# Optimization experiments

Hardware: AMD Instinct MI355X
Metric: run time of the kernel (lower is better)

The kernel has to match this reference:

```python
import jax, jax.numpy as jnp
import numpy as np

N_NODES = 50000   # batch_size * num_nodes
N_EDGES = 800000
D_IN = 128
D_OUT = 128


def setup_inputs() -> dict:
    key = jax.random.key(0)
    k1, k2, k3, k4 = jax.random.split(key, 4)
    x = jax.random.normal(k1, (N_NODES, D_IN), dtype=jnp.float32)
    edge_index = jax.random.randint(k2, (2, N_EDGES), 0, N_NODES, dtype=jnp.int64)
    W = jax.random.normal(k3, (D_OUT, D_IN), dtype=jnp.float32) * (1.0 / np.sqrt(D_IN))
    b = jax.random.normal(k4, (D_OUT,), dtype=jnp.float32) * 0.01
    return {"x": x, "edge_index": edge_index, "batch_size": 50, "num_nodes": 1000, "W": W, "b": b}


def reference(x, edge_index, batch_size, num_nodes, W, b):
    dim_size = batch_size * num_nodes
    row, col = edge_index[0], edge_index[1]
    # gather messages and segment-mean aggregate over destination rows
    msgs = x[col]                                   # [E, D_IN]
    summed = jax.ops.segment_sum(msgs, row, num_segments=dim_size)      # [N, D_IN]
    counts = jax.ops.segment_sum(jnp.ones((row.shape[0],), dtype=x.dtype), row,
                                 num_segments=dim_size)                 # [N]
    mean = summed / jnp.maximum(counts, 1.0)[:, None]                   # 0 for empty rows
    # linear projection (torch Linear: y = x @ W.T + b)
    return mean @ W.T + b
```

## Files before the change

### kernel.cpp

```cpp
#include <hip/hip_runtime.h>

#define D 128
#define BSHIFT 6
#define BCAP 1536
#define EPB_A 2048

typedef unsigned short ushort_t;
typedef unsigned int uint_t;
typedef __attribute__((ext_vector_type(8))) short short8_t;
typedef __attribute__((ext_vector_type(4))) float f32x4_t;

__device__ __forceinline__ bool eidx_is64(const int* eidx) {
    int lane = threadIdx.x & 63;
    int probe = eidx[2 * lane + 1];
    return __ballot(probe != 0) == 0ULL;
}

__device__ __forceinline__ uint_t f2bf(float f) {
    union { float f; uint_t i; } v; v.f = f;
    return (v.i + 0x7fffu + ((v.i >> 16) & 1u)) >> 16;
}
__device__ __forceinline__ float bf_lo(uint_t w) {
    union { uint_t i; float f; } v; v.i = w << 16; return v.f;
}
__device__ __forceinline__ float bf_hi(uint_t w) {
    union { uint_t i; float f; } v; v.i = w & 0xffff0000u; return v.f;
}

__global__ __launch_bounds__(256) void bucketA_kernel(
    const int* __restrict__ eidx, int* __restrict__ gcur,
    int* __restrict__ bucket, int E, int NBUK) {
    __shared__ int lhist[1024];
    __shared__ int lbase[1024];
    bool is64 = eidx_is64(eidx);
    int t = threadIdx.x;
    for (int i = t; i < NBUK; i += 256) lhist[i] = 0;
    __syncthreads();

    int e0 = blockIdx.x * EPB_A;
    int e1 = min(e0 + EPB_A, E);
    for (int e = e0 + t; e < e1; e += 256) {
        int r = is64 ? eidx[2 * e] : eidx[e];
        atomicAdd(&lhist[r >> BSHIFT], 1);
    }
    __syncthreads();
    for (int i = t; i < NBUK; i += 256) {
        int h = lhist[i];
        lbase[i] = (h > 0) ? atomicAdd(&gcur[i], h) : 0;
        lhist[i] = 0;
    }
    __syncthreads();
    for (int e = e0 + t; e < e1; e += 256) {
        int r, c;
        if (is64) { r = eidx[2 * e]; c = eidx[2 * E + 2 * e]; }
        else      { r = eidx[e];     c = eidx[E + e]; }
        int b = r >> BSHIFT;
        int p = atomicAdd(&lhist[b], 1);
        int idx = lbase[b] + p;
        if (idx < BCAP) bucket[b * BCAP + idx] = ((r & 63) << 24) | c;
    }
}

__global__ __launch_bounds__(256) void prep_kernel(
    const int* __restrict__ gcur, const int* __restrict__ bucket,
    int* __restrict__ elist, int* __restrict__ cnt,
    int* __restrict__ start, int N, int NBUK,
    const float* __restrict__ x, uint_t* __restrict__ xb, int total8, int cvb,
    const float* __restrict__ Wsrc, uint_t* __restrict__ wb) {
    __shared__ int lcnt[64], lpos[64], lstart[64];
    int t = threadIdx.x;

    if ((int)blockIdx.x >= NBUK) {
        if (xb == nullptr) return;
        int cb = blockIdx.x - NBUK;
        if (cb < cvb) {
            int i = cb * 256 + t;
            if (i < total8) {
                const float4* p = (const float4*)(x + (size_t)i * 8);
                float4 a = p[0], b = p[1];
                uint4 o;
                o.x = f2bf(a.x) | (f2bf(a.y) << 16);
                o.y = f2bf(a.z) | (f2bf(a.w) << 16);
                o.z = f2bf(b.x) | (f2bf(b.y) << 16);
                o.w = f2bf(b.z) | (f2bf(b.w) << 16);
                *(uint4*)(xb + (size_t)i * 4) = o;
            }
            if (cb == 0 && t < 16) {
                uint4 z; z.x = 0u; z.y = 0u; z.z = 0u; z.w = 0u;
                ((uint4*)(xb + (size_t)N * (D / 2)))[t] = z;
            }
        } else {
            int i = (cb - cvb) * 256 + t;
            if (i < D * D / 8) {
                const float4* p = (const float4*)(Wsrc + (size_t)i * 8);
                float4 a = p[0], b = p[1];
                uint4 o;
                o.x = f2bf(a.x) | (f2bf(a.y) << 16);
                o.y = f2bf(a.z) | (f2bf(a.w) << 16);
                o.z = f2bf(b.x) | (f2bf(b.y) << 16);
                o.w = f2bf(b.z) | (f2bf(b.w) << 16);
                *(uint4*)(wb + (size_t)i * 4) = o;
            }
        }
        return;
    }

    int b = blockIdx.x;
    if (t < 64) { lcnt[t] = 0; lpos[t] = 0; }
    __syncthreads();
    int tot = min(gcur[b], BCAP);
    const int* bp = bucket + (size_t)b * BCAP;
    for (int i = t; i < tot; i += 256)
        atomicAdd(&lcnt[bp[i] >> 24], 1);
    __syncthreads();
    if (t == 0) {
        int run = 0;
        #pragma unroll
        for (int i = 0; i < 64; ++i) {
            lstart[i] = run;
            run += (lcnt[i] + 7) & ~7;
        }
    }
    __syncthreads();
    for (int i = t; i < tot; i += 256) {
        int v = bp[i];
        int rl = v >> 24;
        int p = atomicAdd(&lpos[rl], 1);
        int idx = lstart[rl] + p;
        if (idx < BCAP) elist[(size_t)b * BCAP + idx] = v & 0xFFFFFF;
    }
    if (t < 64) {
        int gr = (b << BSHIFT) + t;
        int c0 = lcnt[t];
        int pe = (c0 + 7) & ~7;
        for (int p = c0; p < pe; ++p) {
            int idx = lstart[t] + p;
            if (idx < BCAP) elist[(size_t)b * BCAP + idx] = N;
        }
        if (gr < N) { cnt[gr] = c0; start[gr] = b * BCAP + lstart[t]; }
    }
}

#define GATHER8(CA, CB)                                                       \
    {                                                                         \
        uint4 g0 = *(const uint4*)(xs + (size_t)(CA).x * D);                  \
        uint4 g1 = *(const uint4*)(xs + (size_t)(CA).y * D);                  \
        uint4 g2 = *(const uint4*)(xs + (size_t)(CA).z * D);                  \
        uint4 g3 = *(const uint4*)(xs + (size_t)(CA).w * D);                  \
        uint4 g4 = *(const uint4*)(xs + (size_t)(CB).x * D);                  \
        uint4 g5 = *(const uint4*)(xs + (size_t)(CB).y * D);                  \
        uint4 g6 = *(const uint4*)(xs + (size_t)(CB).z * D);                  \
        uint4 g7 = *(const uint4*)(xs + (size_t)(CB).w * D);                  \
        a0 += ((bf_lo(g0.x) + bf_lo(g1.x)) + (bf_lo(g2.x) + bf_lo(g3.x)))     \
            + ((bf_lo(g4.x) + bf_lo(g5.x)) + (bf_lo(g6.x) + bf_lo(g7.x)));    \
        a1 += ((bf_hi(g0.x) + bf_hi(g1.x)) + (bf_hi(g2.x) + bf_hi(g3.x)))     \
            + ((bf_hi(g4.x) + bf_hi(g5.x)) + (bf_hi(g6.x) + bf_hi(g7.x)));    \
        a2 += ((bf_lo(g0.y) + bf_lo(g1.y)) + (bf_lo(g2.y) + bf_lo(g3.y)))     \
            + ((bf_lo(g4.y) + bf_lo(g5.y)) + (bf_lo(g6.y) + bf_lo(g7.y)));    \
        a3 += ((bf_hi(g0.y) + bf_hi(g1.y)) + (bf_hi(g2.y) + bf_hi(g3.y)))     \
            + ((bf_hi(g4.y) + bf_hi(g5.y)) + (bf_hi(g6.y) + bf_hi(g7.y)));    \
        a4 += ((bf_lo(g0.z) + bf_lo(g1.z)) + (bf_lo(g2.z) + bf_lo(g3.z)))     \
            + ((bf_lo(g4.z) + bf_lo(g5.z)) + (bf_lo(g6.z) + bf_lo(g7.z)));    \
        a5 += ((bf_hi(g0.z) + bf_hi(g1.z)) + (bf_hi(g2.z) + bf_hi(g3.z)))     \
            + ((bf_hi(g4.z) + bf_hi(g5.z)) + (bf_hi(g6.z) + bf_hi(g7.z)));    \
        a6 += ((bf_lo(g0.w) + bf_lo(g1.w)) + (bf_lo(g2.w) + bf_lo(g3.w)))     \
            + ((bf_lo(g4.w) + bf_lo(g5.w)) + (bf_lo(g6.w) + bf_lo(g7.w)));    \
        a7 += ((bf_hi(g0.w) + bf_hi(g1.w)) + (bf_hi(g2.w) + bf_hi(g3.w)))     \
            + ((bf_hi(g4.w) + bf_hi(g5.w)) + (bf_hi(g6.w) + bf_hi(g7.w)));    \
    }

__global__ __launch_bounds__(256, 6) void fused_bf_kernel(
    const ushort_t* __restrict__ xb, const int* __restrict__ elist,
    const int* __restrict__ cnt, const int* __restrict__ start,
    const ushort_t* __restrict__ Wb, const float* __restrict__ bias,
    float* __restrict__ out, int N) {
    __shared__ ushort_t sA[32 * 136];
    int t = threadIdx.x;
    int lane = t & 63, wave = t >> 6;
    int qr = lane >> 4, sl = lane & 15;
    int nbase = blockIdx.x * 32;
    const ushort_t* xs = xb + 8 * sl;

    #pragma unroll
    for (int quad = 0; quad < 2; ++quad) {
        int n = wave * 8 + quad * 4 + qr;
        int gn = nbase + n;
        int nr  = (gn < N) ? cnt[gn]   : 0;
        int beg = (gn < N) ? start[gn] : 0;
        int nr8 = (nr + 7) & ~7;
        int mn = nr8;
        mn = min(mn, __shfl_xor(mn, 16));
        mn = min(mn, __shfl_xor(mn, 32));
        float a0 = 0.f, a1 = 0.f, a2 = 0.f, a3 = 0.f;
        float a4 = 0.f, a5 = 0.f, a6 = 0.f, a7 = 0.f;
        const int* ep = elist + beg;
        int4 cA, cB;
        if (nr8 > 0) { cA = *(const int4*)ep; cB = *(const int4*)(ep + 4); }
        int i = 0;
        for (; i < mn; ) {
            int ni = i + 8;
            int4 nA2, nB2;
            if (ni < nr8) {
                nA2 = *(const int4*)(ep + ni);
                nB2 = *(const int4*)(ep + ni + 4);
            }
            GATHER8(cA, cB)
            cA = nA2; cB = nB2; i = ni;
        }
        for (; i < nr8; i += 8) {
            int4 dA = *(const int4*)(ep + i);
            int4 dB = *(const int4*)(ep + i + 4);
            GATHER8(dA, dB)
        }
        float inv = (nr > 0) ? 1.0f / (float)nr : 0.0f;
        uint4 pk;
        pk.x = f2bf(a0 * inv) | (f2bf(a1 * inv) << 16);
        pk.y = f2bf(a2 * inv) | (f2bf(a3 * inv) << 16);
        pk.z = f2bf(a4 * inv) | (f2bf(a5 * inv) << 16);
        pk.w = f2bf(a6 * inv) | (f2bf(a7 * inv) << 16);
        *(uint4*)(sA + n * 136 + 8 * sl) = pk;
    }
    __syncthreads();

    {
        int rt = wave & 1, jgrp = wave >> 1;
        int ml = lane & 15, kh = lane >> 4;
        short8_t afr[4];
        #pragma unroll
        for (int ks = 0; ks < 4; ++ks)
            afr[ks] = *(const short8_t*)(sA + (rt * 16 + ml) * 136 + ks * 32 + kh * 8);
        f32x4_t acc[4];
        #pragma unroll
        for (int q = 0; q < 4; ++q) acc[q] = (f32x4_t){0.f, 0.f, 0.f, 0.f};
        #pragma unroll
        for (int q = 0; q < 4; ++q) {
            int j = (jgrp * 4 + q) * 16 + ml;
            #pragma unroll
            for (int ks = 0; ks < 4; ++ks) {
                short8_t bfr = *(const short8_t*)(Wb + (size_t)j * D + ks * 32 + kh * 8);
                acc[q] = __builtin_amdgcn_mfma_f32_16x16x32_bf16(afr[ks], bfr, acc[q], 0, 0, 0);
            }
        }
        #pragma unroll
        for (int q = 0; q < 4; ++q) {
            int j = (jgrp * 4 + q) * 16 + ml;
            float bj = bias[j];
            #pragma unroll
            for (int r = 0; r < 4; ++r) {
                int gn = nbase + rt * 16 + kh * 4 + r;
                if (gn < N) out[(size_t)gn * D + j] = acc[q][r] + bj;
            }
        }
    }
}

__global__ __launch_bounds__(256, 6) void fused_kernel(
    const float* __restrict__ x, const int* __restrict__ elist,
    const int* __restrict__ cnt, const int* __restrict__ start,
    const float* __restrict__ W, const float* __restrict__ bias,
    float* __restrict__ out, int N) {
    __shared__ float sT[128 * 36];
    __shared__ float wc[16 * 132];
    int t = threadIdx.x;
    int lane = t & 63, wave = t >> 6;
    int half = lane >> 5, sl = lane & 31;
    int nbase = blockIdx.x * 32;

    #pragma unroll
    for (int pair = 0; pair < 4; ++pair) {
        int n = wave * 8 + pair * 2 + half;
        int gn = nbase + n;
        int nr  = (gn < N) ? cnt[gn]   : 0;
        int beg = (gn < N) ? start[gn] : 0;
        int nro  = __shfl(nr, lane ^ 32);
        int both = min(nr, nro);
        float ax = 0.f, ay = 0.f, az = 0.f, aw = 0.f;
        int i = 0;
        for (; i + 8 <= both; i += 8) {
            int4 cA = *(const int4*)(elist + beg + i);
            int4 cB = *(const int4*)(elist + beg + i + 4);
            float4 v0 = *(const float4*)(x + (size_t)cA.x * D + 4 * sl);
            float4 v1 = *(const float4*)(x + (size_t)cA.y * D + 4 * sl);
            float4 v2 = *(const float4*)(x + (size_t)cA.z * D + 4 * sl);
            float4 v3 = *(const float4*)(x + (size_t)cA.w * D + 4 * sl);
            float4 v4 = *(const float4*)(x + (size_t)cB.x * D + 4 * sl);
            float4 v5 = *(const float4*)(x + (size_t)cB.y * D + 4 * sl);
            float4 v6 = *(const float4*)(x + (size_t)cB.z * D + 4 * sl);
            float4 v7 = *(const float4*)(x + (size_t)cB.w * D + 4 * sl);
            ax += ((v0.x + v1.x) + (v2.x + v3.x)) + ((v4.x + v5.x) + (v6.x + v7.x));
            ay += ((v0.y + v1.y) + (v2.y + v3.y)) + ((v4.y + v5.y) + (v6.y + v7.y));
            az += ((v0.z + v1.z) + (v2.z + v3.z)) + ((v4.z + v5.z) + (v6.z + v7.z));
            aw += ((v0.w + v1.w) + (v2.w + v3.w)) + ((v4.w + v5.w) + (v6.w + v7.w));
        }
        for (; i < nr; ++i) {
            int c0 = elist[beg + i];
            float4 v = *(const float4*)(x + (size_t)c0 * D + 4 * sl);
            ax += v.x; ay += v.y; az += v.z; aw += v.w;
        }
        float inv = (nr > 0) ? 1.0f / (float)nr : 0.0f;
        int k0 = 4 * sl;
        sT[(k0 + 0) * 36 + n] = ax * inv;
        sT[(k0 + 1) * 36 + n] = ay * inv;
        sT[(k0 + 2) * 36 + n] = az * inv;
        sT[(k0 + 3) * 36 + n] = aw * inv;
    }

    int jg = t & 31, ng = t >> 5;
    int j0 = jg * 4, n0 = ng * 4;
    float acc[4][4] = {};
    for (int kc = 0; kc < 8; ++kc) {
        __syncthreads();
        #pragma unroll
        for (int i = 0; i < 8; ++i) {
            int idx = t + i * 256;
            int j = idx >> 4, kk = idx & 15;
            wc[kk * 132 + j] = W[j * D + kc * 16 + kk];
        }
        __syncthreads();
        #pragma unroll
        for (int kk = 0; kk < 16; ++kk) {
            int k = kc * 16 + kk;
            float4 s4 = *(const float4*)(sT + k * 36 + n0);
            float4 w4 = *(const float4*)(wc + kk * 132 + j0);
            acc[0][0] = fmaf(s4.x, w4.x, acc[0][0]); acc[0][1] = fmaf(s4.x, w4.y, acc[0][1]);
            acc[0][2] = fmaf(s4.x, w4.z, acc[0][2]); acc[0][3] = fmaf(s4.x, w4.w, acc[0][3]);
            acc[1][0] = fmaf(s4.y, w4.x, acc[1][0]); acc[1][1] = fmaf(s4.y, w4.y, acc[1][1]);
            acc[1][2] = fmaf(s4.y, w4.z, acc[1][2]); acc[1][3] = fmaf(s4.y, w4.w, acc[1][3]);
            acc[2][0] = fmaf(s4.z, w4.x, acc[2][0]); acc[2][1] = fmaf(s4.z, w4.y, acc[2][1]);
            acc[2][2] = fmaf(s4.z, w4.z, acc[2][2]); acc[2][3] = fmaf(s4.z, w4.w, acc[2][3]);
            acc[3][0] = fmaf(s4.w, w4.x, acc[3][0]); acc[3][1] = fmaf(s4.w, w4.y, acc[3][1]);
            acc[3][2] = fmaf(s4.w, w4.z, acc[3][2]); acc[3][3] = fmaf(s4.w, w4.w, acc[3][3]);
        }
    }
    float4 b4 = *(const float4*)(bias + j0);
    #pragma unroll
    for (int i = 0; i < 4; ++i) {
        int gn = nbase + n0 + i;
        if (gn >= N) continue;
        float4 o;
        o.x = acc[i][0] + b4.x;
        o.y = acc[i][1] + b4.y;
        o.z = acc[i][2] + b4.z;
        o.w = acc[i][3] + b4.w;
        *(float4*)(out + (size_t)gn * D + j0) = o;
    }
}

__global__ __launch_bounds__(256) void scatter_kernel(
    const float* __restrict__ x, const int* __restrict__ eidx,
    float* summed, float* __restrict__ counts, int E) {
    int t = blockIdx.x * 256 + threadIdx.x;
    int lane = threadIdx.x & 63;
    bool is64 = eidx_is64(eidx);
    int e = t >> 6;
    if (e >= E) return;
    int d = lane * 2;
    int r, c;
    if (is64) { r = eidx[2 * e]; c = eidx[2 * E + 2 * e]; }
    else      { r = eidx[e];     c = eidx[E + e]; }
    float2 v = *(const float2*)(x + (size_t)c * D + d);
    float* dst = summed + (size_t)r * D + d;
    atomicAdd(dst, v.x);
    atomicAdd(dst + 1, v.y);
    if (lane == 0) atomicAdd(counts + r, 1.0f);
}

__global__ __launch_bounds__(256) void divide_kernel(
    float* __restrict__ sums, const float* __restrict__ counts, int N) {
    int g = blockIdx.x * 256 + threadIdx.x;
    int r = g >> 6, lane = g & 63;
    if (r >= N) return;
    float inv = 1.0f / fmaxf(counts[r], 1.0f);
    float2* p = (float2*)(sums + (size_t)r * D + 2 * lane);
    float2 v = *p;
    v.x *= inv; v.y *= inv;
    *p = v;
}

__global__ __launch_bounds__(256) void gemm_kernel(
    float* inout, const float* __restrict__ W,
    const float* __restrict__ bias, int N) {
    __shared__ float sT[128 * 36];
    __shared__ float wc[32 * 132];
    int t = threadIdx.x;
    int nbase = blockIdx.x * 32;
    #pragma unroll
    for (int i = 0; i < 16; ++i) {
        int idx = t + i * 256;
        int n = idx >> 7, k = idx & 127;
        int gn = nbase + n;
        sT[k * 36 + n] = (gn < N) ? inout[(size_t)gn * D + k] : 0.0f;
    }
    int jg = t & 31, ng = t >> 5;
    int j0 = jg * 4, n0 = ng * 4;
    float acc[4][4] = {};
    for (int kc = 0; kc < 4; ++kc) {
        __syncthreads();
        #pragma unroll
        for (int i = 0; i < 16; ++i) {
            int idx = t + i * 256;
            int j = idx >> 5, kk = idx & 31;
            wc[kk * 132 + j] = W[j * D + kc * 32 + kk];
        }
        __syncthreads();
        #pragma unroll 8
        for (int kk = 0; kk < 32; ++kk) {
            int k = kc * 32 + kk;
            float4 s4 = *(const float4*)(sT + k * 36 + n0);
            float4 w4 = *(const float4*)(wc + kk * 132 + j0);
            acc[0][0] = fmaf(s4.x, w4.x, acc[0][0]); acc[0][1] = fmaf(s4.x, w4.y, acc[0][1]);
            acc[0][2] = fmaf(s4.x, w4.z, acc[0][2]); acc[0][3] = fmaf(s4.x, w4.w, acc[0][3]);
            acc[1][0] = fmaf(s4.y, w4.x, acc[1][0]); acc[1][1] = fmaf(s4.y, w4.y, acc[1][1]);
            acc[1][2] = fmaf(s4.y, w4.z, acc[1][2]); acc[1][3] = fmaf(s4.y, w4.w, acc[1][3]);
            acc[2][0] = fmaf(s4.z, w4.x, acc[2][0]); acc[2][1] = fmaf(s4.z, w4.y, acc[2][1]);
            acc[2][2] = fmaf(s4.z, w4.z, acc[2][2]); acc[2][3] = fmaf(s4.z, w4.w, acc[2][3]);
            acc[3][0] = fmaf(s4.w, w4.x, acc[3][0]); acc[3][1] = fmaf(s4.w, w4.y, acc[3][1]);
            acc[3][2] = fmaf(s4.w, w4.z, acc[3][2]); acc[3][3] = fmaf(s4.w, w4.w, acc[3][3]);
        }
    }
    float4 b4 = *(const float4*)(bias + j0);
    #pragma unroll
    for (int i = 0; i < 4; ++i) {
        int gn = nbase + n0 + i;
        if (gn >= N) continue;
        float4 o;
        o.x = acc[i][0] + b4.x;
        o.y = acc[i][1] + b4.y;
        o.z = acc[i][2] + b4.z;
        o.w = acc[i][3] + b4.w;
        *(float4*)(inout + (size_t)gn * D + j0) = o;
    }
}

extern "C" void kernel_launch(void* const* d_in, const int* in_sizes, int n_in,
                              void* d_out, int out_size, void* d_ws, size_t ws_size,
                              hipStream_t stream) {
    const float* x = (const float*)d_in[0];
    const int* eidx = (const int*)d_in[1];
    const float* W = (const float*)d_in[4];
    const float* b = (const float*)d_in[5];
    float* out = (float*)d_out;

    int N = in_sizes[0] / D;
    int E = in_sizes[1] / 2;
    int NBUK = (N + 63) >> BSHIFT;
    int fb = (N + 31) / 32;
    int ab = (E + EPB_A - 1) / EPB_A;

    size_t o0 = 0;
    size_t o_gc = o0;  o0 += ((size_t)NBUK * 4 + 255) & ~255ULL;
    size_t o_cn = o0;  o0 += ((size_t)N * 4 + 255) & ~255ULL;
    size_t o_st = o0;  o0 += ((size_t)N * 4 + 255) & ~255ULL;
    size_t o_bk = o0;  o0 += (size_t)NBUK * BCAP * 4;
    size_t o_el = o0;  o0 += (size_t)NBUK * BCAP * 4;
    size_t base_need = o0;
    size_t o_xb = o0;  o0 += (((size_t)(N + 1) * D * 2) + 255) & ~255ULL;
    size_t o_wb = o0;  size_t bf_need = o0 + (size_t)D * D * 2;

    bool cap_ok = (N <= 65536) && ((size_t)NBUK * BCAP >= (size_t)E);

    int cvb = (N * D / 8 + 255) / 256;
    int wvb = (D * D / 8 + 255) / 256;

    if (cap_ok && ws_size >= bf_need) {
        char* ws = (char*)d_ws;
        int*      gcur  = (int*)(ws + o_gc);
        int*      cnt   = (int*)(ws + o_cn);
        int*      start = (int*)(ws + o_st);
        int*      bkt   = (int*)(ws + o_bk);
        int*      elist = (int*)(ws + o_el);
        ushort_t* xb    = (ushort_t*)(ws + o_xb);
        ushort_t* wb    = (ushort_t*)(ws + o_wb);

        hipMemsetAsync(gcur, 0, (size_t)NBUK * 4, stream);
        bucketA_kernel<<<ab, 256, 0, stream>>>(eidx, gcur, bkt, E, NBUK);
        prep_kernel<<<NBUK + cvb + wvb, 256, 0, stream>>>(
            gcur, bkt, elist, cnt, start, N, NBUK,
            x, (uint_t*)xb, N * D / 8, cvb, W, (uint_t*)wb);
        fused_bf_kernel<<<fb, 256, 0, stream>>>(xb, elist, cnt, start, wb, b, out, N);
    } else if (cap_ok && ws_size >= base_need) {
        char* ws = (char*)d_ws;
        int* gcur  = (int*)(ws + o_gc);
        int* cnt   = (int*)(ws + o_cn);
        int* start = (int*)(ws + o_st);
        int* bkt   = (int*)(ws + o_bk);
        int* elist = (int*)(ws + o_el);

        hipMemsetAsync(gcur, 0, (size_t)NBUK * 4, stream);
        bucketA_kernel<<<ab, 256, 0, stream>>>(eidx, gcur, bkt, E, NBUK);
        prep_kernel<<<NBUK, 256, 0, stream>>>(
            gcur, bkt, elist, cnt, start, N, NBUK,
            nullptr, nullptr, 0, 0, nullptr, nullptr);
        fused_kernel<<<fb, 256, 0, stream>>>(x, elist, cnt, start, W, b, out, N);
    } else {
        float* counts = (float*)d_ws;
        hipMemsetAsync(d_out, 0, (size_t)N * D * sizeof(float), stream);
        hipMemsetAsync(d_ws, 0, (size_t)N * sizeof(float), stream);
        int sb = (E * 64 + 255) / 256;
        scatter_kernel<<<sb, 256, 0, stream>>>(x, eidx, out, counts, E);
        int db = (N * 64 + 255) / 256;
        divide_kernel<<<db, 256, 0, stream>>>(out, counts, N);
        gemm_kernel<<<fb, 256, 0, stream>>>(out, W, b, N);
    }
}
```

Measured before the change: 164.5 us.

## Widen gather to 16 edges per iteration and cache edge indices in bucketing

The aggregation loop now gathers 16 neighbor rows per iteration instead of 8, with a per-lane prefetch of the next 16 indices. The launch-bounds occupancy hint drops from 6 to 3 to make room for the extra registers. The bucketing kernel loads each block's row/col indices once into registers, replacing the second global read. The goal is more memory-level parallelism in the gather and less index traffic, at the cost of lower occupancy and per-lane divergence, since the wave-wide min loop is removed.

```diff
diff --git a/kernel.cpp b/kernel.cpp
--- a/kernel.cpp
+++ b/kernel.cpp
@@ -39,9 +39,16 @@
 
     int e0 = blockIdx.x * EPB_A;
     int e1 = min(e0 + EPB_A, E);
-    for (int e = e0 + t; e < e1; e += 256) {
-        int r = is64 ? eidx[2 * e] : eidx[e];
-        atomicAdd(&lhist[r >> BSHIFT], 1);
+    int rr[8], cc[8];
+    #pragma unroll
+    for (int k = 0; k < 8; ++k) {
+        int e = e0 + t + k * 256;
+        rr[k] = -1;
+        if (e < e1) {
+            if (is64) { rr[k] = eidx[2 * e]; cc[k] = eidx[2 * E + 2 * e]; }
+            else      { rr[k] = eidx[e];     cc[k] = eidx[E + e]; }
+            atomicAdd(&lhist[rr[k] >> BSHIFT], 1);
+        }
     }
     __syncthreads();
     for (int i = t; i < NBUK; i += 256) {
@@ -50,14 +57,14 @@
         lhist[i] = 0;
     }
     __syncthreads();
-    for (int e = e0 + t; e < e1; e += 256) {
-        int r, c;
-        if (is64) { r = eidx[2 * e]; c = eidx[2 * E + 2 * e]; }
-        else      { r = eidx[e];     c = eidx[E + e]; }
-        int b = r >> BSHIFT;
-        int p = atomicAdd(&lhist[b], 1);
-        int idx = lbase[b] + p;
-        if (idx < BCAP) bucket[b * BCAP + idx] = ((r & 63) << 24) | c;
+    #pragma unroll
+    for (int k = 0; k < 8; ++k) {
+        if (rr[k] >= 0) {
+            int b = rr[k] >> BSHIFT;
+            int p = atomicAdd(&lhist[b], 1);
+            int idx = lbase[b] + p;
+            if (idx < BCAP) bucket[b * BCAP + idx] = ((rr[k] & 63) << 24) | cc[k];
+        }
     }
 }
 
@@ -169,7 +176,59 @@
             + ((bf_hi(g4.w) + bf_hi(g5.w)) + (bf_hi(g6.w) + bf_hi(g7.w)));    \
     }
 
-__global__ __launch_bounds__(256, 6) void fused_bf_kernel(
+#define GATHER16(CA, CB, CC, CD)                                              \
+    {                                                                         \
+        uint4 g0 = *(const uint4*)(xs + (size_t)(CA).x * D);                  \
+        uint4 g1 = *(const uint4*)(xs + (size_t)(CA).y * D);                  \
+        uint4 g2 = *(const uint4*)(xs + (size_t)(CA).z * D);                  \
+        uint4 g3 = *(const uint4*)(xs + (size_t)(CA).w * D);                  \
+        uint4 g4 = *(const uint4*)(xs + (size_t)(CB).x * D);                  \
+        uint4 g5 = *(const uint4*)(xs + (size_t)(CB).y * D);                  \
+        uint4 g6 = *(const uint4*)(xs + (size_t)(CB).z * D);                  \
+        uint4 g7 = *(const uint4*)(xs + (size_t)(CB).w * D);                  \
+        uint4 g8 = *(const uint4*)(xs + (size_t)(CC).x * D);                  \
+        uint4 g9 = *(const uint4*)(xs + (size_t)(CC).y * D);                  \
+        uint4 ga = *(const uint4*)(xs + (size_t)(CC).z * D);                  \
+        uint4 gb = *(const uint4*)(xs + (size_t)(CC).w * D);                  \
+        uint4 gc = *(const uint4*)(xs + (size_t)(CD).x * D);                  \
+        uint4 gd = *(const uint4*)(xs + (size_t)(CD).y * D);                  \
+        uint4 ge = *(const uint4*)(xs + (size_t)(CD).z * D);                  \
+        uint4 gf = *(const uint4*)(xs + (size_t)(CD).w * D);                  \
+        a0 += (((bf_lo(g0.x) + bf_lo(g1.x)) + (bf_lo(g2.x) + bf_lo(g3.x)))    \
+             + ((bf_lo(g4.x) + bf_lo(g5.x)) + (bf_lo(g6.x) + bf_lo(g7.x))))   \
+            + (((bf_lo(g8.x) + bf_lo(g9.x)) + (bf_lo(ga.x) + bf_lo(gb.x)))    \
+             + ((bf_lo(gc.x) + bf_lo(gd.x)) + (bf_lo(ge.x) + bf_lo(gf.x))));  \
+        a1 += (((bf_hi(g0.x) + bf_hi(g1.x)) + (bf_hi(g2.x) + bf_hi(g3.x)))    \
+             + ((bf_hi(g4.x) + bf_hi(g5.x)) + (bf_hi(g6.x) + bf_hi(g7.x))))   \
+            + (((bf_hi(g8.x) + bf_hi(g9.x)) + (bf_hi(ga.x) + bf_hi(gb.x)))    \
+             + ((bf_hi(gc.x) + bf_hi(gd.x)) + (bf_hi(ge.x) + bf_hi(gf.x))));  \
+        a2 += (((bf_lo(g0.y) + bf_lo(g1.y)) + (bf_lo(g2.y) + bf_lo(g3.y)))    \
+             + ((bf_lo(g4.y) + bf_lo(g5.y)) + (bf_lo(g6.y) + bf_lo(g7.y))))   \
+            + (((bf_lo(g8.y) + bf_lo(g9.y)) + (bf_lo(ga.y) + bf_lo(gb.y)))    \
+             + ((bf_lo(gc.y) + bf_lo(gd.y)) + (bf_lo(ge.y) + bf_lo(gf.y))));  \
+        a3 += (((bf_hi(g0.y) + bf_hi(g1.y)) + (bf_hi(g2.y) + bf_hi(g3.y)))    \
+             + ((bf_hi(g4.y) + bf_hi(g5.y)) + (bf_hi(g6.y) + bf_hi(g7.y))))   \
+            + (((bf_hi(g8.y) + bf_hi(g9.y)) + (bf_hi(ga.y) + bf_hi(gb.y)))    \
+             + ((bf_hi(gc.y) + bf_hi(gd.y)) + (bf_hi(ge.y) + bf_hi(gf.y))));  \
+        a4 += (((bf_lo(g0.z) + bf_lo(g1.z)) + (bf_lo(g2.z) + bf_lo(g3.z)))    \
+             + ((bf_lo(g4.z) + bf_lo(g5.z)) + (bf_lo(g6.z) + bf_lo(g7.z))))   \
+            + (((bf_lo(g8.z) + bf_lo(g9.z)) + (bf_lo(ga.z) + bf_lo(gb.z)))    \
+             + ((bf_lo(gc.z) + bf_lo(gd.z)) + (bf_lo(ge.z) + bf_lo(gf.z))));  \
+        a5 += (((bf_hi(g0.z) + bf_hi(g1.z)) + (bf_hi(g2.z) + bf_hi(g3.z)))    \
+             + ((bf_hi(g4.z) + bf_hi(g5.z)) + (bf_hi(g6.z) + bf_hi(g7.z))))   \
+            + (((bf_hi(g8.z) + bf_hi(g9.z)) + (bf_hi(ga.z) + bf_hi(gb.z)))    \
+             + ((bf_hi(gc.z) + bf_hi(gd.z)) + (bf_hi(ge.z) + bf_hi(gf.z))));  \
+        a6 += (((bf_lo(g0.w) + bf_lo(g1.w)) + (bf_lo(g2.w) + bf_lo(g3.w)))    \
+             + ((bf_lo(g4.w) + bf_lo(g5.w)) + (bf_lo(g6.w) + bf_lo(g7.w))))   \
+            + (((bf_lo(g8.w) + bf_lo(g9.w)) + (bf_lo(ga.w) + bf_lo(gb.w)))    \
+             + ((bf_lo(gc.w) + bf_lo(gd.w)) + (bf_lo(ge.w) + bf_lo(gf.w))));  \
+        a7 += (((bf_hi(g0.w) + bf_hi(g1.w)) + (bf_hi(g2.w) + bf_hi(g3.w)))    \
+             + ((bf_hi(g4.w) + bf_hi(g5.w)) + (bf_hi(g6.w) + bf_hi(g7.w))))   \
+            + (((bf_hi(g8.w) + bf_hi(g9.w)) + (bf_hi(ga.w) + bf_hi(gb.w)))    \
+             + ((bf_hi(gc.w) + bf_hi(gd.w)) + (bf_hi(ge.w) + bf_hi(gf.w))));  \
+    }
+
+__global__ __launch_bounds__(256, 3) void fused_bf_kernel(
     const ushort_t* __restrict__ xb, const int* __restrict__ elist,
     const int* __restrict__ cnt, const int* __restrict__ start,
     const ushort_t* __restrict__ Wb, const float* __restrict__ bias,
@@ -188,26 +247,27 @@
         int nr  = (gn < N) ? cnt[gn]   : 0;
         int beg = (gn < N) ? start[gn] : 0;
         int nr8 = (nr + 7) & ~7;
-        int mn = nr8;
-        mn = min(mn, __shfl_xor(mn, 16));
-        mn = min(mn, __shfl_xor(mn, 32));
         float a0 = 0.f, a1 = 0.f, a2 = 0.f, a3 = 0.f;
         float a4 = 0.f, a5 = 0.f, a6 = 0.f, a7 = 0.f;
         const int* ep = elist + beg;
-        int4 cA, cB;
-        if (nr8 > 0) { cA = *(const int4*)ep; cB = *(const int4*)(ep + 4); }
+        int4 cA = make_int4(0, 0, 0, 0), cB = cA, cC = cA, cD = cA;
+        if (16 <= nr8) {
+            cA = *(const int4*)(ep);      cB = *(const int4*)(ep + 4);
+            cC = *(const int4*)(ep + 8);  cD = *(const int4*)(ep + 12);
+        }
         int i = 0;
-        for (; i < mn; ) {
-            int ni = i + 8;
-            int4 nA2, nB2;
-            if (ni < nr8) {
-                nA2 = *(const int4*)(ep + ni);
-                nB2 = *(const int4*)(ep + ni + 4);
+        while (i + 16 <= nr8) {
+            int ni = i + 16;
+            int4 nA = cA, nB = cB, nC = cC, nD = cD;
+            if (ni + 16 <= nr8) {
+                nA = *(const int4*)(ep + ni);      nB = *(const int4*)(ep + ni + 4);
+                nC = *(const int4*)(ep + ni + 8);  nD = *(const int4*)(ep + ni + 12);
             }
-            GATHER8(cA, cB)
-            cA = nA2; cB = nB2; i = ni;
-        }
-        for (; i < nr8; i += 8) {
+            GATHER16(cA, cB, cC, cD)
+            cA = nA; cB = nB; cC = nC; cD = nD;
+            i = ni;
+        }
+        if (i + 8 <= nr8) {
             int4 dA = *(const int4*)(ep + i);
             int4 dB = *(const int4*)(ep + i + 4);
             GATHER8(dA, dB)
```

New measurement: 157.4 us. 1.05x faster.
